# Optimization experiments

Measured on AMD Instinct MI355X. Metric: run time of the kernel, lower is better.

The kernel has to match this reference:

```python
import jax, jax.numpy as jnp
import numpy as np

B, L, NB = 8192, 40, 2        # batch, maxlen, behavior features
V, E = 100000, 64             # vocab per table, embed dim per table
NS, ND = 3, 8                 # other sparse feats, dense feats
D = NB * E                    # concatenated behavior embed dim = 128
ALL = D + D + (ND + NS * E)   # info_all dim = 456
NEG_INF = -2.0**32 + 1
BN_EPS = 1e-3                 # keras BatchNormalization default epsilon


def setup_inputs() -> dict:
    key = jax.random.key(0)
    ks = jax.random.split(key, 20)
    inp = {
        "dense_inputs": jax.random.normal(ks[0], (B, ND), jnp.float32),
        "sparse_inputs": jax.random.randint(ks[1], (B, NS), 0, V),
        "seq_inputs": jax.random.randint(ks[2], (B, L, NB), 0, V),
        "item_inputs": jax.random.randint(ks[3], (B, NB), 0, V),
        # embedding tables (random_uniform init in keras)
        "emb_sparse": jax.random.uniform(ks[4], (NS, V, E), jnp.float32, -0.05, 0.05),
        "emb_seq": jax.random.uniform(ks[5], (NB, V, E), jnp.float32, -0.05, 0.05),
        # attention MLP: input 4*D=512 -> 80 -> 40 -> 1
        "att_W1": jax.random.normal(ks[6], (4 * D, 80), jnp.float32) * 0.05,
        "att_b1": jnp.zeros((80,), jnp.float32),
        "att_W2": jax.random.normal(ks[7], (80, 40), jnp.float32) * 0.05,
        "att_b2": jnp.zeros((40,), jnp.float32),
        "att_Wf": jax.random.normal(ks[8], (40, 1), jnp.float32) * 0.05,
        "att_bf": jnp.zeros((1,), jnp.float32),
        # batch norm (inference-mode moving stats)
        "bn_gamma": jnp.ones((ALL,), jnp.float32),
        "bn_beta": jnp.zeros((ALL,), jnp.float32),
        "bn_mean": jnp.zeros((ALL,), jnp.float32),
        "bn_var": jnp.ones((ALL,), jnp.float32),
        # FFN: ALL -> 80 -> 40 -> 1, PReLU alphas per-feature
        "ffn_W1": jax.random.normal(ks[9], (ALL, 80), jnp.float32) * 0.05,
        "ffn_b1": jnp.zeros((80,), jnp.float32),
        "ffn_a1": jnp.full((80,), 0.25, jnp.float32),
        "ffn_W2": jax.random.normal(ks[10], (80, 40), jnp.float32) * 0.05,
        "ffn_b2": jnp.zeros((40,), jnp.float32),
        "ffn_a2": jnp.full((40,), 0.25, jnp.float32),
        "out_W": jax.random.normal(ks[11], (40, 1), jnp.float32) * 0.05,
        "out_b": jnp.zeros((1,), jnp.float32),
    }
    return inp


def prelu(x, alpha):
    return jnp.where(x > 0, x, alpha * x)


def reference(dense_inputs, sparse_inputs, seq_inputs, item_inputs,
              emb_sparse, emb_seq,
              att_W1, att_b1, att_W2, att_b2, att_Wf, att_bf,
              bn_gamma, bn_beta, bn_mean, bn_var,
              ffn_W1, ffn_b1, ffn_a1, ffn_W2, ffn_b2, ffn_a2,
              out_W, out_b):
    mask = (seq_inputs[:, :, 0] != 0)                                   # [B, L]
    # other sparse embeddings + dense features
    other_info = jnp.concatenate(
        [dense_inputs] + [emb_sparse[i][sparse_inputs[:, i]] for i in range(NS)], axis=-1)
    # behavior sequence / candidate item embeddings
    seq_embed = jnp.concatenate([emb_seq[i][seq_inputs[:, :, i]] for i in range(NB)], axis=-1)  # [B,L,D]
    item_embed = jnp.concatenate([emb_seq[i][item_inputs[:, i]] for i in range(NB)], axis=-1)   # [B,D]

    # local activation attention
    q = jnp.broadcast_to(item_embed[:, None, :], seq_embed.shape)       # [B,L,D]
    info = jnp.concatenate([q, seq_embed, q - seq_embed, q * seq_embed], axis=-1)  # [B,L,4D]
    h = jax.nn.sigmoid(info @ att_W1 + att_b1)
    h = jax.nn.sigmoid(h @ att_W2 + att_b2)
    logits = (h @ att_Wf + att_bf)[..., 0]                               # [B,L]
    logits = jnp.where(mask, logits, NEG_INF)
    att = jax.nn.softmax(logits, axis=-1)                                # [B,L]
    user_info = jnp.einsum('bl,bld->bd', att, seq_embed)                 # [B,D]

    info_all = jnp.concatenate([user_info, item_embed, other_info], axis=-1)  # [B,ALL]
    info_all = bn_gamma * (info_all - bn_mean) * jax.lax.rsqrt(bn_var + BN_EPS) + bn_beta
    info_all = prelu(info_all @ ffn_W1 + ffn_b1, ffn_a1)
    info_all = prelu(info_all @ ffn_W2 + ffn_b2, ffn_a2)
    return jax.nn.sigmoid(info_all @ out_W + out_b)                      # [B,1]
```

## Files before the change

### kernel.cpp

```cpp
#include <hip/hip_runtime.h>

#define BB 8192
#define LL 40
#define VV 100000
#define NEG_INF_F (-4294967295.0f)
#define XS 136
#define HS 104
#define XGS 480

typedef __attribute__((ext_vector_type(8))) short short8;
typedef __attribute__((ext_vector_type(4))) float f32x4;

__device__ __forceinline__ unsigned short f2bf(float f) {
  unsigned u = __float_as_uint(f);
  u += 0x7FFFu + ((u >> 16) & 1u);
  return (unsigned short)(u >> 16);
}
__device__ __forceinline__ float bf2f(unsigned short s) {
  return __uint_as_float(((unsigned)s) << 16);
}

__device__ __forceinline__ short8 fuseB(short8 wsd, short8 wd, float4 qa, float4 qb) {
  float qv[8] = {qa.x, qa.y, qa.z, qa.w, qb.x, qb.y, qb.z, qb.w};
  short8 o;
#pragma unroll
  for (int j = 0; j < 8; j++)
    o[j] = (short)f2bf(bf2f((unsigned short)wsd[j]) + qv[j] * bf2f((unsigned short)wd[j]));
  return o;
}

__global__ void prep_all(const float* __restrict__ W1, float* __restrict__ wqcT,
                         unsigned short* __restrict__ WsdpT,
                         const float* __restrict__ aW2, unsigned short* __restrict__ W2bT,
                         const float* __restrict__ fW2, unsigned short* __restrict__ W2fT,
                         const float* __restrict__ fW1, const float* __restrict__ g,
                         const float* __restrict__ vr, unsigned short* __restrict__ W1fT,
                         const float* __restrict__ fb1, const float* __restrict__ be,
                         const float* __restrict__ mn, float* __restrict__ b1p) {
  __shared__ float red[4];
  int bid = blockIdx.x, t = threadIdx.x;
  if (bid < 40) {
    int i = bid * 256 + t;
    int h = i >> 7, k = i & 127;
    float a = W1[k * 80 + h];
    float b = W1[(128 + k) * 80 + h];
    float c = W1[(256 + k) * 80 + h];
    float d = W1[(384 + k) * 80 + h];
    wqcT[h * 132 + k] = a + c;
    WsdpT[h * 256 + k] = f2bf(b - c);
    WsdpT[h * 256 + 128 + k] = f2bf(d);
  } else if (bid < 58) {
    int i = (bid - 40) * 256 + t;
    int n = i / 96, k = i % 96;
    W2bT[i] = (n < 40 && k < 80) ? f2bf(aW2[k * 40 + n]) : (unsigned short)0;
  } else if (bid < 76) {
    int i = (bid - 58) * 256 + t;
    int n = i / 96, k = i % 96;
    W2fT[i] = (n < 40 && k < 80) ? f2bf(fW2[k * 40 + n]) : (unsigned short)0;
  } else if (bid < 226) {
    int i = (bid - 76) * 256 + t;
    int n = i / 480, k = i % 480;
    float v = 0.f;
    if (k < 456) v = fW1[k * 80 + n] * g[k] * rsqrtf(vr[k] + 1e-3f);
    W1fT[i] = f2bf(v);
  } else {
    int n = bid - 226;
    float p = 0.f;
    for (int k = t; k < 456; k += 256) {
      float sc = g[k] * rsqrtf(vr[k] + 1e-3f);
      p += (be[k] - mn[k] * sc) * fW1[k * 80 + n];
    }
    for (int off = 32; off; off >>= 1) p += __shfl_xor(p, off, 64);
    if ((t & 63) == 0) red[t >> 6] = p;
    __syncthreads();
    if (t == 0) b1p[n] = fb1[n] + red[0] + red[1] + red[2] + red[3];
  }
}


__launch_bounds__(256, 6)
__global__ void din_att(const float* __restrict__ dense, const int* __restrict__ sparsei,
                        const int* __restrict__ seqi, const int* __restrict__ itemi,
                        const float* __restrict__ embS, const float* __restrict__ embQ,
                        const float* __restrict__ wqcT, const unsigned short* __restrict__ WsdpT,
                        const unsigned short* __restrict__ W2bT,
                        const float* __restrict__ ab1, const float* __restrict__ ab2,
                        const float* __restrict__ aWf, const float* __restrict__ abf,
                        unsigned short* __restrict__ Xg) {
  __shared__ __align__(16) char smem[21632];
  unsigned short* sX  = (unsigned short*)smem;
  unsigned short* sH1 = (unsigned short*)(smem + 10880);
  float* sQ     = (float*)(smem + 19200);
  float* sQCp   = sQ + 128;
  float* sOther = sQCp + 160;
  float* sAtt   = sOther + 200;
  float* sLogit = sAtt + 40;
  float* sMask  = sLogit + 40;

  const int t = threadIdx.x;
  const int b = blockIdx.x;
  const int wv = t >> 6, ln = t & 63, m16 = ln & 15, quad = ln >> 4;

  if (t < 32) {
    int f = t >> 4, sub = t & 15;
    int idx = itemi[b * 2 + f];
    float4 v = *(const float4*)(embQ + ((size_t)(f * VV + idx)) * 64 + sub * 4);
    *(float4*)(sQ + f * 64 + sub * 4) = v;
  } else if (t < 80) {
    int j = t - 32, f = j >> 4, sub = j & 15;
    int idx = sparsei[b * 3 + f];
    float4 v = *(const float4*)(embS + ((size_t)(f * VV + idx)) * 64 + sub * 4);
    *(float4*)(sOther + 8 + f * 64 + sub * 4) = v;
  } else if (t < 88) {
    sOther[t - 80] = dense[b * 8 + (t - 80)];
  } else if (t < 128) {
    sLogit[t - 88] = 0.f;
  }
  for (int i = t; i < 1280; i += 256) {
    int r = i >> 4, sub = i & 15;
    int l = r >> 1, f = r & 1;
    int idx = seqi[b * 80 + r];
    float4 v = *(const float4*)(embQ + ((size_t)(f * VV + idx)) * 64 + sub * 4);
    ushort4 u;
    u.x = f2bf(v.x); u.y = f2bf(v.y); u.z = f2bf(v.z); u.w = f2bf(v.w);
    *(ushort4*)(sX + l * XS + f * 64 + sub * 4) = u;
    if (((r & 1) | sub) == 0) sMask[l] = (idx != 0) ? 0.f : NEG_INF_F;
  }
  for (int i = t; i < 320; i += 256) {
    int r = i >> 3, c = i & 7;
    ((unsigned*)sH1)[r * 52 + 40 + c] = 0u;
  }
  __syncthreads();

  if (t < 160) {
    int h = (t < 80) ? t : t - 80;
    int k0 = (t < 80) ? 0 : 64;
    float acc = (t < 80) ? ab1[h] : 0.f;
    const float* wq = wqcT + h * 132 + k0;
    const float* qq = sQ + k0;
    for (int k = 0; k < 64; k += 4) {
      float4 w = *(const float4*)(wq + k);
      float4 q = *(const float4*)(qq + k);
      acc += q.x * w.x + q.y * w.y + q.z * w.z + q.w * w.w;
    }
    sQCp[t] = acc;
  }
  short8 Bp[4];
  {
    const unsigned short* br = WsdpT + (size_t)(wv * 16 + m16) * 256 + quad * 8;
#pragma unroll
    for (int kt = 0; kt < 4; kt++) {
      short8 w1 = *(const short8*)(br + kt * 32);
      short8 w2 = *(const short8*)(br + 128 + kt * 32);
      int k0 = quad * 8 + kt * 32;
      Bp[kt] = fuseB(w1, w2, *(const float4*)(sQ + k0), *(const float4*)(sQ + k0 + 4));
    }
  }
  __syncthreads();

  {
    const int h = wv * 16 + m16;
    const float qc = sQCp[h] + sQCp[80 + h];
#pragma unroll
    for (int mt = 0; mt < 3; mt++) {
      f32x4 acc = {0.f, 0.f, 0.f, 0.f};
      const unsigned short* ar = sX + (mt * 16 + m16) * XS + quad * 8;
#pragma unroll
      for (int kt = 0; kt < 4; kt++) {
        short8 a = *(const short8*)(ar + kt * 32);
        acc = __builtin_amdgcn_mfma_f32_16x16x32_bf16(a, Bp[kt], acc, 0, 0, 0);
      }
#pragma unroll
      for (int r = 0; r < 4; r++) {
        int l = mt * 16 + quad * 4 + r;
        if (l < 40) {
          float z = acc[r] + qc;
          sH1[l * HS + h] = f2bf(1.f / (1.f + __expf(-z)));
        }
      }
    }
    if (wv < 3) {
      const unsigned short* br = WsdpT + (size_t)(64 + m16) * 256 + quad * 8;
      const unsigned short* ar = sX + (wv * 16 + m16) * XS + quad * 8;
      f32x4 acc = {0.f, 0.f, 0.f, 0.f};
#pragma unroll
      for (int kt = 0; kt < 4; kt++) {
        short8 w1 = *(const short8*)(br + kt * 32);
        short8 w2 = *(const short8*)(br + 128 + kt * 32);
        int k0 = quad * 8 + kt * 32;
        short8 bp = fuseB(w1, w2, *(const float4*)(sQ + k0), *(const float4*)(sQ + k0 + 4));
        short8 a = *(const short8*)(ar + kt * 32);
        acc = __builtin_amdgcn_mfma_f32_16x16x32_bf16(a, bp, acc, 0, 0, 0);
      }
      int h4 = 64 + m16;
      float qc4 = sQCp[h4] + sQCp[80 + h4];
#pragma unroll
      for (int r = 0; r < 4; r++) {
        int l = wv * 16 + quad * 4 + r;
        if (l < 40) {
          float z = acc[r] + qc4;
          sH1[l * HS + h4] = f2bf(1.f / (1.f + __expf(-z)));
        }
      }
    }
  }
  __syncthreads();

  for (int tile = wv; tile < 9; tile += 4) {
    int mt = tile / 3, nt = tile % 3;
    f32x4 acc = {0.f, 0.f, 0.f, 0.f};
    const unsigned short* ar = sH1 + (mt * 16 + m16) * HS + quad * 8;
    const unsigned short* br = W2bT + (nt * 16 + m16) * 96 + quad * 8;
#pragma unroll
    for (int kt = 0; kt < 3; kt++) {
      short8 a = *(const short8*)(ar + kt * 32);
      short8 bb = *(const short8*)(br + kt * 32);
      acc = __builtin_amdgcn_mfma_f32_16x16x32_bf16(a, bb, acc, 0, 0, 0);
    }
    int j = nt * 16 + m16;
    float b2 = (j < 40) ? ab2[j] : 0.f;
    float wf = (j < 40) ? aWf[j] : 0.f;
    float c[4];
#pragma unroll
    for (int r = 0; r < 4; r++) {
      float h2 = 1.f / (1.f + __expf(-(acc[r] + b2)));
      c[r] = (j < 40) ? h2 * wf : 0.f;
    }
#pragma unroll
    for (int off = 1; off < 16; off <<= 1) {
#pragma unroll
      for (int r = 0; r < 4; r++) c[r] += __shfl_xor(c[r], off, 64);
    }
    if (m16 == 0) {
#pragma unroll
      for (int r = 0; r < 4; r++) {
        int l = mt * 16 + quad * 4 + r;
        if (l < 40) atomicAdd(&sLogit[l], c[r]);
      }
    }
  }
  __syncthreads();

  if (wv == 0) {
    float logit = -3.0e38f;
    if (t < 40) logit = sLogit[t] + abf[0] + sMask[t];
    float mx = logit;
    for (int off = 32; off; off >>= 1) mx = fmaxf(mx, __shfl_xor(mx, off, 64));
    float ex = (t < 40) ? __expf(logit - mx) : 0.f;
    float sm = ex;
    for (int off = 32; off; off >>= 1) sm += __shfl_xor(sm, off, 64);
    if (t < 40) sAtt[t] = ex / sm;
  } else {
    int j = t - 64;
    unsigned* xr = (unsigned*)(Xg + (size_t)b * XGS);
    if (j < 64) {
      xr[64 + j] = (unsigned)f2bf(sQ[2 * j]) | ((unsigned)f2bf(sQ[2 * j + 1]) << 16);
    } else if (j < 164) {
      int p = j - 64;
      xr[128 + p] = (unsigned)f2bf(sOther[2 * p]) | ((unsigned)f2bf(sOther[2 * p + 1]) << 16);
    } else if (j < 176) {
      xr[228 + (j - 164)] = 0u;
    }
  }
  __syncthreads();

  if (t < 128) {
    float acc = 0.f;
    for (int l = 0; l < 40; l++) acc += sAtt[l] * bf2f(sX[l * XS + t]);
    Xg[(size_t)b * XGS + t] = f2bf(acc);
  }
}


__launch_bounds__(256, 2)
__global__ void din_ffn(const unsigned short* __restrict__ Xg,
                        const unsigned short* __restrict__ W1fT, const float* __restrict__ b1p,
                        const float* __restrict__ fa1,
                        const unsigned short* __restrict__ W2fT, const float* __restrict__ fb2,
                        const float* __restrict__ fa2,
                        const float* __restrict__ oW, const float* __restrict__ ob,
                        float* __restrict__ out) {
  __shared__ __align__(16) unsigned short sXB[16 * 488];
  __shared__ __align__(16) unsigned short sH1B[16 * HS];
  __shared__ float sH2B[16 * 41];
  const int t = threadIdx.x, blk = blockIdx.x;
  const int wv = t >> 6, ln = t & 63, m16 = ln & 15, quad = ln >> 4;

  short8 Bf[15];
  {
    const unsigned short* br = W1fT + (size_t)(wv * 16 + m16) * 480 + quad * 8;
#pragma unroll
    for (int kt = 0; kt < 15; kt++) Bf[kt] = *(const short8*)(br + kt * 32);
  }

  for (int i = t; i < 960; i += 256) {
    int r = i / 60, c = i % 60;
    *(uint4*)(sXB + r * 488 + c * 8) =
        *(const uint4*)(Xg + (size_t)(blk * 16 + r) * XGS + c * 8);
  }
  if (t < 128) {
    int r = t >> 3, c = t & 7;
    ((unsigned*)sH1B)[r * 52 + 40 + c] = 0u;
  }
  __syncthreads();

  {
    int h = wv * 16 + m16;
    f32x4 acc = {0.f, 0.f, 0.f, 0.f};
    const unsigned short* ar = sXB + m16 * 488 + quad * 8;
#pragma unroll
    for (int kt = 0; kt < 15; kt++) {
      short8 a = *(const short8*)(ar + kt * 32);
      acc = __builtin_amdgcn_mfma_f32_16x16x32_bf16(a, Bf[kt], acc, 0, 0, 0);
    }
    float b1v = b1p[h], a1v = fa1[h];
#pragma unroll
    for (int r = 0; r < 4; r++) {
      int l = quad * 4 + r;
      float z = acc[r] + b1v;
      z = z > 0.f ? z : a1v * z;
      sH1B[l * HS + h] = f2bf(z);
    }
    if (wv == 0) {
      short8 B4[15];
      const unsigned short* br = W1fT + (size_t)(64 + m16) * 480 + quad * 8;
#pragma unroll
      for (int kt = 0; kt < 15; kt++) B4[kt] = *(const short8*)(br + kt * 32);
      f32x4 acc4 = {0.f, 0.f, 0.f, 0.f};
#pragma unroll
      for (int kt = 0; kt < 15; kt++) {
        short8 a = *(const short8*)(ar + kt * 32);
        acc4 = __builtin_amdgcn_mfma_f32_16x16x32_bf16(a, B4[kt], acc4, 0, 0, 0);
      }
      int h4 = 64 + m16;
      float b1v4 = b1p[h4], a1v4 = fa1[h4];
#pragma unroll
      for (int r = 0; r < 4; r++) {
        int l = quad * 4 + r;
        float z = acc4[r] + b1v4;
        z = z > 0.f ? z : a1v4 * z;
        sH1B[l * HS + h4] = f2bf(z);
      }
    }
  }
  __syncthreads();

  if (wv < 3) {
    f32x4 acc = {0.f, 0.f, 0.f, 0.f};
    const unsigned short* ar = sH1B + m16 * HS + quad * 8;
    const unsigned short* br = W2fT + (wv * 16 + m16) * 96 + quad * 8;
#pragma unroll
    for (int kt = 0; kt < 3; kt++) {
      short8 a = *(const short8*)(ar + kt * 32);
      short8 bb = *(const short8*)(br + kt * 32);
      acc = __builtin_amdgcn_mfma_f32_16x16x32_bf16(a, bb, acc, 0, 0, 0);
    }
    int j = wv * 16 + m16;
    if (j < 40) {
      float b2 = fb2[j], a2 = fa2[j];
#pragma unroll
      for (int r = 0; r < 4; r++) {
        int l = quad * 4 + r;
        float z = acc[r] + b2;
        sH2B[l * 41 + j] = z > 0.f ? z : a2 * z;
      }
    }
  }
  __syncthreads();

  if (t < 16) {
    float acc = ob[0];
    for (int j = 0; j < 40; j++) acc += sH2B[t * 41 + j] * oW[j];
    out[blk * 16 + t] = 1.f / (1.f + __expf(-acc));
  }
}


extern "C" void kernel_launch(void* const* d_in, const int* in_sizes, int n_in,
                              void* d_out, int out_size, void* d_ws, size_t ws_size,
                              hipStream_t stream) {
  const float* dense  = (const float*)d_in[0];
  const int*   sparsei = (const int*)d_in[1];
  const int*   seqi   = (const int*)d_in[2];
  const int*   itemi  = (const int*)d_in[3];
  const float* embS   = (const float*)d_in[4];
  const float* embQ   = (const float*)d_in[5];
  const float* aW1    = (const float*)d_in[6];
  const float* ab1    = (const float*)d_in[7];
  const float* aW2    = (const float*)d_in[8];
  const float* ab2    = (const float*)d_in[9];
  const float* aWf    = (const float*)d_in[10];
  const float* abf    = (const float*)d_in[11];
  const float* bng    = (const float*)d_in[12];
  const float* bnb    = (const float*)d_in[13];
  const float* bnm    = (const float*)d_in[14];
  const float* bnv    = (const float*)d_in[15];
  const float* fW1    = (const float*)d_in[16];
  const float* fb1    = (const float*)d_in[17];
  const float* fa1    = (const float*)d_in[18];
  const float* fW2    = (const float*)d_in[19];
  const float* fb2    = (const float*)d_in[20];
  const float* fa2    = (const float*)d_in[21];
  const float* oW     = (const float*)d_in[22];
  const float* ob     = (const float*)d_in[23];
  float* out = (float*)d_out;

  float* ws = (float*)d_ws;
  float* wqcT = ws;
  float* b1p  = ws + 10560;
  unsigned short* WsdpT = (unsigned short*)(ws + 10640);
  unsigned short* W2bT  = (unsigned short*)(ws + 20880);
  unsigned short* W2fT  = (unsigned short*)(ws + 23184);
  unsigned short* W1fT  = (unsigned short*)(ws + 25488);
  unsigned short* Xg    = (unsigned short*)(ws + 44688);

  prep_all<<<306, 256, 0, stream>>>(aW1, wqcT, WsdpT, aW2, W2bT, fW2, W2fT,
                                    fW1, bng, bnv, W1fT, fb1, bnb, bnm, b1p);
  din_att<<<BB, 256, 0, stream>>>(dense, sparsei, seqi, itemi, embS, embQ,
                                  wqcT, WsdpT, W2bT, ab1, ab2, aWf, abf, Xg);
  din_ffn<<<512, 256, 0, stream>>>(Xg, W1fT, b1p, fa1, W2fT, fb2, fa2, oW, ob, out);
}
```

Baseline: 316.1 us.

## Use hardware bf16 pack, fast reciprocal sigmoid, direct Xg writes, and higher occupancy

Replaces the software bf16 rounding with the v_cvt_pk_bf16_f32 instruction and packs pairs of values. Sigmoid and softmax normalisation now use the fast reciprocal builtin. Item, sparse and dense features are written to the global Xg row as soon as they are gathered, so the late copy phase and its shared buffers go away; shared memory shrinks and the launch bound rises from 6 to 8 blocks. The query-constant dot product moves to 80 threads with two accumulators, and padded A rows are clamped to row 39. Rounding and NaN behaviour may differ slightly from the software conversion, and the higher block count tightens the register budget.

After: 320.8 us. About the same (+1.5%).

```diff
diff --git a/kernel.cpp b/kernel.cpp
--- a/kernel.cpp
+++ b/kernel.cpp
@@ -11,22 +11,33 @@
 typedef __attribute__((ext_vector_type(8))) short short8;
 typedef __attribute__((ext_vector_type(4))) float f32x4;
 
+__device__ __forceinline__ unsigned cvt_pk_bf16(float a, float b) {
+  unsigned r;
+  asm("v_cvt_pk_bf16_f32 %0, %1, %2" : "=v"(r) : "v"(a), "v"(b));
+  return r;
+}
 __device__ __forceinline__ unsigned short f2bf(float f) {
-  unsigned u = __float_as_uint(f);
-  u += 0x7FFFu + ((u >> 16) & 1u);
-  return (unsigned short)(u >> 16);
+  return (unsigned short)cvt_pk_bf16(f, f);
 }
 __device__ __forceinline__ float bf2f(unsigned short s) {
   return __uint_as_float(((unsigned)s) << 16);
 }
+__device__ __forceinline__ float sigm(float z) {
+  return __builtin_amdgcn_rcpf(1.f + __expf(-z));
+}
 
 __device__ __forceinline__ short8 fuseB(short8 wsd, short8 wd, float4 qa, float4 qb) {
   float qv[8] = {qa.x, qa.y, qa.z, qa.w, qb.x, qb.y, qb.z, qb.w};
-  short8 o;
+  float f[8];
 #pragma unroll
   for (int j = 0; j < 8; j++)
-    o[j] = (short)f2bf(bf2f((unsigned short)wsd[j]) + qv[j] * bf2f((unsigned short)wd[j]));
-  return o;
+    f[j] = bf2f((unsigned short)wsd[j]) + qv[j] * bf2f((unsigned short)wd[j]);
+  uint4 o;
+  o.x = cvt_pk_bf16(f[0], f[1]);
+  o.y = cvt_pk_bf16(f[2], f[3]);
+  o.z = cvt_pk_bf16(f[4], f[5]);
+  o.w = cvt_pk_bf16(f[6], f[7]);
+  return __builtin_bit_cast(short8, o);
 }
 
 __global__ void prep_all(const float* __restrict__ W1, float* __restrict__ wqcT,
@@ -78,7 +89,7 @@
 }
 
 
-__launch_bounds__(256, 6)
+__launch_bounds__(256, 8)
 __global__ void din_att(const float* __restrict__ dense, const int* __restrict__ sparsei,
                         const int* __restrict__ seqi, const int* __restrict__ itemi,
                         const float* __restrict__ embS, const float* __restrict__ embQ,
@@ -87,43 +98,52 @@
                         const float* __restrict__ ab1, const float* __restrict__ ab2,
                         const float* __restrict__ aWf, const float* __restrict__ abf,
                         unsigned short* __restrict__ Xg) {
-  __shared__ __align__(16) char smem[21632];
+  __shared__ __align__(16) char smem[20352];
   unsigned short* sX  = (unsigned short*)smem;
   unsigned short* sH1 = (unsigned short*)(smem + 10880);
-  float* sQ     = (float*)(smem + 19200);
-  float* sQCp   = sQ + 128;
-  float* sOther = sQCp + 160;
-  float* sAtt   = sOther + 200;
-  float* sLogit = sAtt + 40;
-  float* sMask  = sLogit + 40;
+  float* sQ    = (float*)(smem + 19200);
+  float* sQCp  = sQ + 128;
+  float* sLA   = sQCp + 80;
+  float* sMask = sLA + 40;
 
   const int t = threadIdx.x;
   const int b = blockIdx.x;
   const int wv = t >> 6, ln = t & 63, m16 = ln & 15, quad = ln >> 4;
+  unsigned short* xrow = Xg + (size_t)b * XGS;
 
   if (t < 32) {
     int f = t >> 4, sub = t & 15;
     int idx = itemi[b * 2 + f];
     float4 v = *(const float4*)(embQ + ((size_t)(f * VV + idx)) * 64 + sub * 4);
     *(float4*)(sQ + f * 64 + sub * 4) = v;
+    uint2 p;
+    p.x = cvt_pk_bf16(v.x, v.y);
+    p.y = cvt_pk_bf16(v.z, v.w);
+    *(uint2*)(xrow + 128 + f * 64 + sub * 4) = p;
   } else if (t < 80) {
     int j = t - 32, f = j >> 4, sub = j & 15;
     int idx = sparsei[b * 3 + f];
     float4 v = *(const float4*)(embS + ((size_t)(f * VV + idx)) * 64 + sub * 4);
-    *(float4*)(sOther + 8 + f * 64 + sub * 4) = v;
+    uint2 p;
+    p.x = cvt_pk_bf16(v.x, v.y);
+    p.y = cvt_pk_bf16(v.z, v.w);
+    *(uint2*)(xrow + 264 + f * 64 + sub * 4) = p;
   } else if (t < 88) {
-    sOther[t - 80] = dense[b * 8 + (t - 80)];
-  } else if (t < 128) {
-    sLogit[t - 88] = 0.f;
+    xrow[256 + (t - 80)] = f2bf(dense[b * 8 + (t - 80)]);
+  } else if (t < 100) {
+    ((unsigned*)xrow)[228 + (t - 88)] = 0u;
+  } else if (t < 140) {
+    sLA[t - 100] = 0.f;
   }
   for (int i = t; i < 1280; i += 256) {
     int r = i >> 4, sub = i & 15;
     int l = r >> 1, f = r & 1;
     int idx = seqi[b * 80 + r];
     float4 v = *(const float4*)(embQ + ((size_t)(f * VV + idx)) * 64 + sub * 4);
-    ushort4 u;
-    u.x = f2bf(v.x); u.y = f2bf(v.y); u.z = f2bf(v.z); u.w = f2bf(v.w);
-    *(ushort4*)(sX + l * XS + f * 64 + sub * 4) = u;
+    uint2 p;
+    p.x = cvt_pk_bf16(v.x, v.y);
+    p.y = cvt_pk_bf16(v.z, v.w);
+    *(uint2*)(sX + l * XS + f * 64 + sub * 4) = p;
     if (((r & 1) | sub) == 0) sMask[l] = (idx != 0) ? 0.f : NEG_INF_F;
   }
   for (int i = t; i < 320; i += 256) {
@@ -132,18 +152,18 @@
   }
   __syncthreads();
 
-  if (t < 160) {
-    int h = (t < 80) ? t : t - 80;
-    int k0 = (t < 80) ? 0 : 64;
-    float acc = (t < 80) ? ab1[h] : 0.f;
-    const float* wq = wqcT + h * 132 + k0;
-    const float* qq = sQ + k0;
-    for (int k = 0; k < 64; k += 4) {
-      float4 w = *(const float4*)(wq + k);
-      float4 q = *(const float4*)(qq + k);
-      acc += q.x * w.x + q.y * w.y + q.z * w.z + q.w * w.w;
-    }
-    sQCp[t] = acc;
+  if (t < 80) {
+    float acc0 = ab1[t], acc1 = 0.f;
+    const float* wq = wqcT + t * 132;
+    for (int k = 0; k < 128; k += 8) {
+      float4 w0 = *(const float4*)(wq + k);
+      float4 w1 = *(const float4*)(wq + k + 4);
+      float4 q0 = *(const float4*)(sQ + k);
+      float4 q1 = *(const float4*)(sQ + k + 4);
+      acc0 += q0.x * w0.x + q0.y * w0.y + q0.z * w0.z + q0.w * w0.w;
+      acc1 += q1.x * w1.x + q1.y * w1.y + q1.z * w1.z + q1.w * w1.w;
+    }
+    sQCp[t] = acc0 + acc1;
   }
   short8 Bp[4];
   {
@@ -160,7 +180,7 @@
 
   {
     const int h = wv * 16 + m16;
-    const float qc = sQCp[h] + sQCp[80 + h];
+    const float qc = sQCp[h];
 #pragma unroll
     for (int mt = 0; mt < 3; mt++) {
       f32x4 acc = {0.f, 0.f, 0.f, 0.f};
@@ -170,13 +190,15 @@
         short8 a = *(const short8*)(ar + kt * 32);
         acc = __builtin_amdgcn_mfma_f32_16x16x32_bf16(a, Bp[kt], acc, 0, 0, 0);
       }
-#pragma unroll
-      for (int r = 0; r < 4; r++) {
-        int l = mt * 16 + quad * 4 + r;
-        if (l < 40) {
-          float z = acc[r] + qc;
-          sH1[l * HS + h] = f2bf(1.f / (1.f + __expf(-z)));
-        }
+      float s0 = sigm(acc[0] + qc), s1 = sigm(acc[1] + qc);
+      float s2 = sigm(acc[2] + qc), s3 = sigm(acc[3] + qc);
+      unsigned p01 = cvt_pk_bf16(s0, s1), p23 = cvt_pk_bf16(s2, s3);
+      int l0 = mt * 16 + quad * 4;
+      if (l0 < 40) {
+        sH1[(l0 + 0) * HS + h] = (unsigned short)p01;
+        sH1[(l0 + 1) * HS + h] = (unsigned short)(p01 >> 16);
+        sH1[(l0 + 2) * HS + h] = (unsigned short)p23;
+        sH1[(l0 + 3) * HS + h] = (unsigned short)(p23 >> 16);
       }
     }
     if (wv < 3) {
@@ -193,14 +215,16 @@
         acc = __builtin_amdgcn_mfma_f32_16x16x32_bf16(a, bp, acc, 0, 0, 0);
       }
       int h4 = 64 + m16;
-      float qc4 = sQCp[h4] + sQCp[80 + h4];
-#pragma unroll
-      for (int r = 0; r < 4; r++) {
-        int l = wv * 16 + quad * 4 + r;
-        if (l < 40) {
-          float z = acc[r] + qc4;
-          sH1[l * HS + h4] = f2bf(1.f / (1.f + __expf(-z)));
-        }
+      float qc4 = sQCp[h4];
+      float s0 = sigm(acc[0] + qc4), s1 = sigm(acc[1] + qc4);
+      float s2 = sigm(acc[2] + qc4), s3 = sigm(acc[3] + qc4);
+      unsigned p01 = cvt_pk_bf16(s0, s1), p23 = cvt_pk_bf16(s2, s3);
+      int l0 = wv * 16 + quad * 4;
+      if (l0 < 40) {
+        sH1[(l0 + 0) * HS + h4] = (unsigned short)p01;
+        sH1[(l0 + 1) * HS + h4] = (unsigned short)(p01 >> 16);
+        sH1[(l0 + 2) * HS + h4] = (unsigned short)p23;
+        sH1[(l0 + 3) * HS + h4] = (unsigned short)(p23 >> 16);
       }
     }
   }
@@ -209,7 +233,9 @@
   for (int tile = wv; tile < 9; tile += 4) {
     int mt = tile / 3, nt = tile % 3;
     f32x4 acc = {0.f, 0.f, 0.f, 0.f};
-    const unsigned short* ar = sH1 + (mt * 16 + m16) * HS + quad * 8;
+    int arow = mt * 16 + m16;
+    if (arow > 39) arow = 39;
+    const unsigned short* ar = sH1 + arow * HS + quad * 8;
     const unsigned short* br = W2bT + (nt * 16 + m16) * 96 + quad * 8;
 #pragma unroll
     for (int kt = 0; kt < 3; kt++) {
@@ -223,7 +249,7 @@
     float c[4];
 #pragma unroll
     for (int r = 0; r < 4; r++) {
-      float h2 = 1.f / (1.f + __expf(-(acc[r] + b2)));
+      float h2 = sigm(acc[r] + b2);
       c[r] = (j < 40) ? h2 * wf : 0.f;
     }
 #pragma unroll
@@ -235,7 +261,7 @@
 #pragma unroll
       for (int r = 0; r < 4; r++) {
         int l = mt * 16 + quad * 4 + r;
-        if (l < 40) atomicAdd(&sLogit[l], c[r]);
+        if (l < 40) atomicAdd(&sLA[l], c[r]);
       }
     }
   }
@@ -243,31 +269,20 @@
 
   if (wv == 0) {
     float logit = -3.0e38f;
-    if (t < 40) logit = sLogit[t] + abf[0] + sMask[t];
+    if (t < 40) logit = sLA[t] + abf[0] + sMask[t];
     float mx = logit;
     for (int off = 32; off; off >>= 1) mx = fmaxf(mx, __shfl_xor(mx, off, 64));
     float ex = (t < 40) ? __expf(logit - mx) : 0.f;
     float sm = ex;
     for (int off = 32; off; off >>= 1) sm += __shfl_xor(sm, off, 64);
-    if (t < 40) sAtt[t] = ex / sm;
-  } else {
-    int j = t - 64;
-    unsigned* xr = (unsigned*)(Xg + (size_t)b * XGS);
-    if (j < 64) {
-      xr[64 + j] = (unsigned)f2bf(sQ[2 * j]) | ((unsigned)f2bf(sQ[2 * j + 1]) << 16);
-    } else if (j < 164) {
-      int p = j - 64;
-      xr[128 + p] = (unsigned)f2bf(sOther[2 * p]) | ((unsigned)f2bf(sOther[2 * p + 1]) << 16);
-    } else if (j < 176) {
-      xr[228 + (j - 164)] = 0u;
-    }
+    if (t < 40) sLA[t] = ex * __builtin_amdgcn_rcpf(sm);
   }
   __syncthreads();
 
   if (t < 128) {
     float acc = 0.f;
-    for (int l = 0; l < 40; l++) acc += sAtt[l] * bf2f(sX[l * XS + t]);
-    Xg[(size_t)b * XGS + t] = f2bf(acc);
+    for (int l = 0; l < 40; l++) acc += sLA[l] * bf2f(sX[l * XS + t]);
+    xrow[t] = f2bf(acc);
   }
 }
 
@@ -314,13 +329,17 @@
       acc = __builtin_amdgcn_mfma_f32_16x16x32_bf16(a, Bf[kt], acc, 0, 0, 0);
     }
     float b1v = b1p[h], a1v = fa1[h];
-#pragma unroll
-    for (int r = 0; r < 4; r++) {
-      int l = quad * 4 + r;
-      float z = acc[r] + b1v;
-      z = z > 0.f ? z : a1v * z;
-      sH1B[l * HS + h] = f2bf(z);
-    }
+    float z0 = acc[0] + b1v, z1 = acc[1] + b1v, z2 = acc[2] + b1v, z3 = acc[3] + b1v;
+    z0 = z0 > 0.f ? z0 : a1v * z0;
+    z1 = z1 > 0.f ? z1 : a1v * z1;
+    z2 = z2 > 0.f ? z2 : a1v * z2;
+    z3 = z3 > 0.f ? z3 : a1v * z3;
+    unsigned p01 = cvt_pk_bf16(z0, z1), p23 = cvt_pk_bf16(z2, z3);
+    int l0 = quad * 4;
+    sH1B[(l0 + 0) * HS + h] = (unsigned short)p01;
+    sH1B[(l0 + 1) * HS + h] = (unsigned short)(p01 >> 16);
+    sH1B[(l0 + 2) * HS + h] = (unsigned short)p23;
+    sH1B[(l0 + 3) * HS + h] = (unsigned short)(p23 >> 16);
     if (wv == 0) {
       short8 B4[15];
       const unsigned short* br = W1fT + (size_t)(64 + m16) * 480 + quad * 8;
@@ -334,13 +353,16 @@
       }
       int h4 = 64 + m16;
       float b1v4 = b1p[h4], a1v4 = fa1[h4];
-#pragma unroll
-      for (int r = 0; r < 4; r++) {
-        int l = quad * 4 + r;
-        float z = acc4[r] + b1v4;
-        z = z > 0.f ? z : a1v4 * z;
-        sH1B[l * HS + h4] = f2bf(z);
-      }
+      float y0 = acc4[0] + b1v4, y1 = acc4[1] + b1v4, y2 = acc4[2] + b1v4, y3 = acc4[3] + b1v4;
+      y0 = y0 > 0.f ? y0 : a1v4 * y0;
+      y1 = y1 > 0.f ? y1 : a1v4 * y1;
+      y2 = y2 > 0.f ? y2 : a1v4 * y2;
+      y3 = y3 > 0.f ? y3 : a1v4 * y3;
+      unsigned q01 = cvt_pk_bf16(y0, y1), q23 = cvt_pk_bf16(y2, y3);
+      sH1B[(l0 + 0) * HS + h4] = (unsigned short)q01;
+      sH1B[(l0 + 1) * HS + h4] = (unsigned short)(q01 >> 16);
+      sH1B[(l0 + 2) * HS + h4] = (unsigned short)q23;
+      sH1B[(l0 + 3) * HS + h4] = (unsigned short)(q23 >> 16);
     }
   }
   __syncthreads();
@@ -371,7 +393,7 @@
   if (t < 16) {
     float acc = ob[0];
     for (int j = 0; j < 40; j++) acc += sH2B[t * 41 + j] * oW[j];
-    out[blk * 16 + t] = 1.f / (1.f + __expf(-acc));
+    out[blk * 16 + t] = sigm(acc);
   }
 }
 
```
